# Optimization experiments

Hardware: AMD Instinct MI355X
Metric: run time of the kernel (lower is better)

The kernel has to match this reference:

```python
import jax, jax.numpy as jnp
import numpy as np

N = 262144   # faces = edges = vertices
E = 2000000  # connections per bipartite edge set
W = 32       # out_width


def _linear_block(x, w, b):
    # LinearBlock(in, out) with defaults -> Linear + LeakyReLU(0.01)
    return jax.nn.leaky_relu(x @ w + b)


def _bip_res_mr_conv(x_src, x_dst, e, w, b):
    # diffs = x_dst[e1] - x_src[e0]; scatter_max over dst; MLP(cat) residual
    diffs = x_dst[e[1]] - x_src[e[0]]                       # [E, W]
    maxes = jax.ops.segment_max(diffs, e[1], num_segments=x_dst.shape[0])
    # torch_scatter.scatter_max fills empty slots with 0
    maxes = jnp.where(jnp.isfinite(maxes), maxes, 0.0)
    h = _linear_block(jnp.concatenate([x_dst, maxes], axis=1), w, b)
    return x_dst + h


def setup_inputs() -> dict:
    key = jax.random.key(0)
    ks = jax.random.split(key, 16)
    inp = {
        "x_f": jax.random.normal(ks[0], (N, 4), dtype=jnp.float32),
        "x_e": jax.random.normal(ks[1], (N, 6), dtype=jnp.float32),
        "x_v": jax.random.normal(ks[2], (N, 3), dtype=jnp.float32),
        "e_fe": jax.random.randint(ks[3], (2, E), 0, N),
        "e_ev": jax.random.randint(ks[4], (2, E), 0, N),
        "e_ef": jax.random.randint(ks[5], (2, E), 0, N),
        "e_ve": jax.random.randint(ks[6], (2, E), 0, N),
    }
    def lin(k, cin, cout):
        s = 1.0 / np.sqrt(cin)
        kw, kb = jax.random.split(k)
        return (jax.random.uniform(kw, (cin, cout), minval=-s, maxval=s, dtype=jnp.float32),
                jax.random.uniform(kb, (cout,), minval=-s, maxval=s, dtype=jnp.float32))
    inp["wf"], inp["bf"] = lin(ks[7], 4, W)
    inp["we"], inp["be"] = lin(ks[8], 6, W)
    inp["wv"], inp["bv"] = lin(ks[9], 3, W)
    inp["w_f2e"], inp["b_f2e"] = lin(ks[10], 2 * W, W)
    inp["w_e2v"], inp["b_e2v"] = lin(ks[11], 2 * W, W)   # E2V conv
    return inp


def reference(x_f, x_e, x_v, e_fe, e_ev, e_ef, e_ve,
              wf, bf, we, be, wv, bv, w_f2e, b_f2e, w_e2v, b_e2v):
    x_f = _linear_block(x_f, wf, bf)
    x_e = _linear_block(x_e, we, be)
    x_v = _linear_block(x_v, wv, bv)
    # NB: original forward reuses self.F2E weights for three convs
    x_e = _bip_res_mr_conv(x_f, x_e, e_fe, w_f2e, b_f2e)
    x_v = _bip_res_mr_conv(x_e, x_v, e_ev, w_e2v, b_e2v)
    x_f = _bip_res_mr_conv(x_e, x_f, e_ef, w_f2e, b_f2e)
    x_e = _bip_res_mr_conv(x_v, x_e, e_ve, w_f2e, b_f2e)
    return (x_f, x_e, x_v)
```

## Files before the change

kernel.cpp:

```cpp
#include <hip/hip_runtime.h>
#include <hip/hip_fp16.h>
#include <math.h>

#define N_NODES 262144
#define NE      2000000
#define W_OUT   32

#define NBINS          2048
#define BIN_SHIFT      7
#define NPB            128
#define CAP            1200
#define MROW           33
#define MXU_DW         ((((NPB + 1) * MROW) + 3) & ~3)

__device__ __forceinline__ float lrelu(float x) { return x >= 0.f ? x : 0.01f * x; }

__device__ __forceinline__ unsigned short key16f(float r) {
    unsigned short u = __half_as_ushort(__float2half(r));
    return (u & 0x8000u) ? (unsigned short)(~u) : (unsigned short)(u | 0x8000u);
}
__device__ __forceinline__ float unkey16(unsigned k) {
    unsigned bits = (k & 0x8000u) ? (k ^ 0x8000u) : ((~k) & 0xFFFFu);
    return __half2float(__ushort_as_half((unsigned short)bits));
}
__device__ __forceinline__ unsigned fmin_key(float f) {
    unsigned u = __float_as_uint(f);
    return (u & 0x80000000u) ? ~u : (u | 0x80000000u);
}
__device__ __forceinline__ float fmin_unkey(unsigned u) {
    return __uint_as_float((u & 0x80000000u) ? (u ^ 0x80000000u) : ~u);
}

template<int K>
__global__ void proj_kernel(const float* __restrict__ x, const float* __restrict__ w,
                            const float* __restrict__ b, float* __restrict__ out,
                            unsigned short* __restrict__ out_k) {
    __shared__ float wl[K * 32];
    __shared__ float xl[8 * K];
    int t = threadIdx.x;
    for (int i = t; i < K * 32; i += 256) wl[i] = w[i];
    int nbase = blockIdx.x * 8;
    for (int i = t; i < 8 * K; i += 256) xl[i] = x[nbase * K + i];
    __syncthreads();
    int j = t & 31, ln = t >> 5;
    float acc = b[j];
#pragma unroll
    for (int k = 0; k < K; ++k) acc += xl[ln * K + k] * wl[k * 32 + j];
    float r = lrelu(acc);
    out[nbase * 32 + t] = r;
    if (out_k) out_k[nbase * 32 + t] = key16f(r);
}

__global__ __launch_bounds__(512)
void bin_pass3(const int* __restrict__ e0, const int* __restrict__ e1,
               int* __restrict__ gcur, unsigned int* __restrict__ buckets) {
    __shared__ unsigned int hist[NBINS];
    __shared__ unsigned int lcur[NBINS];
    __shared__ unsigned int gbase[NBINS];
    int t = threadIdx.x;
    for (int i = t; i < NBINS; i += 512) hist[i] = 0;
    __syncthreads();

    int q0 = blockIdx.x * 2048 + t;
    int4 d4[4];
#pragma unroll
    for (int k = 0; k < 4; ++k) {
        int q = q0 + k * 512;
        if (q < NE / 4) {
            d4[k] = ((const int4*)e1)[q];
            atomicAdd(&hist[((unsigned)d4[k].x) >> BIN_SHIFT], 1u);
            atomicAdd(&hist[((unsigned)d4[k].y) >> BIN_SHIFT], 1u);
            atomicAdd(&hist[((unsigned)d4[k].z) >> BIN_SHIFT], 1u);
            atomicAdd(&hist[((unsigned)d4[k].w) >> BIN_SHIFT], 1u);
        }
    }
    __syncthreads();
    for (int i = t; i < NBINS; i += 512) {
        lcur[i] = 0;
        if (hist[i]) gbase[i] = atomicAdd((unsigned int*)&gcur[i], hist[i]);
    }
    __syncthreads();
#pragma unroll
    for (int k = 0; k < 4; ++k) {
        int q = q0 + k * 512;
        if (q < NE / 4) {
            int4 s4 = ((const int4*)e0)[q];
            const int ds[4] = {d4[k].x, d4[k].y, d4[k].z, d4[k].w};
            const int ss[4] = {s4.x, s4.y, s4.z, s4.w};
#pragma unroll
            for (int j = 0; j < 4; ++j) {
                unsigned d = (unsigned)ds[j];
                unsigned bin = d >> BIN_SHIFT;
                unsigned pos = gbase[bin] + atomicAdd(&lcur[bin], 1u);
                if (pos < CAP)
                    buckets[(size_t)bin * CAP + pos] =
                        ((d & (NPB - 1u)) << 18) | (unsigned)ss[j];
            }
        }
    }
}

template<bool H>
__global__ __launch_bounds__(256)
void binreduce9(const int* __restrict__ gcur, const unsigned int* __restrict__ buckets,
                const void* __restrict__ srcv, const float* __restrict__ dst,
                const float* __restrict__ w, const float* __restrict__ b,
                float* __restrict__ out, unsigned short* __restrict__ out_k) {
    __shared__ unsigned mxu[MXU_DW];
    __shared__ __align__(16) float4 wl4[16 * 32];
    __shared__ __align__(16) float xmat[8][2][64];
    int t = threadIdx.x;
    int bin = blockIdx.x;
    int hw = t >> 5, c = t & 31;

    uint4* m4 = (uint4*)mxu;
    for (int i = t; i < MXU_DW / 4; i += 256)
        m4[i] = make_uint4(0xFFFFFFFFu, 0xFFFFFFFFu, 0xFFFFFFFFu, 0xFFFFFFFFu);
    for (int i = t; i < 512; i += 256) {
        int k4 = i >> 5, cc = i & 31;
        wl4[i] = make_float4(w[(k4 * 4 + 0) * 32 + cc], w[(k4 * 4 + 1) * 32 + cc],
                             w[(k4 * 4 + 2) * 32 + cc], w[(k4 * 4 + 3) * 32 + cc]);
    }
    __syncthreads();

    int nb = min(gcur[bin], CAP);
    const unsigned int* bk = buckets + (size_t)bin * CAP;
    const unsigned SENT = (unsigned)NPB << 18;
    const unsigned short* sk = (const unsigned short*)srcv;
    const float* sf = (const float*)srcv;
    for (int cbase = hw * 32; cbase < nb; cbase += 256) {
        int idx = cbase + c;
        unsigned ent = (idx < nb) ? bk[idx] : SENT;
#pragma unroll
        for (int k0 = 0; k0 < 32; k0 += 8) {
            unsigned v[8], nd[8];
#pragma unroll
            for (int j = 0; j < 8; ++j) {
                unsigned e = __shfl(ent, k0 + j, 32);
                nd[j] = e >> 18;
                size_t off = (size_t)(e & 0x3FFFFu) * 32 + c;
                if (H) v[j] = (unsigned)sk[off];
                else   v[j] = fmin_key(sf[off]);
            }
#pragma unroll
            for (int j = 0; j < 8; ++j)
                atomicMin(&mxu[nd[j] * MROW + c], v[j]);
        }
    }
    __syncthreads();

    float bc = b[c];
    size_t gb = (size_t)bin * NPB;
    for (int grp = 0; grp < 8; ++grp) {
        int n0 = hw * 16 + grp * 2;
#pragma unroll
        for (int gg = 0; gg < 2; ++gg) {
            int node = n0 + gg;
            float dv = dst[(gb + node) * 32 + c];
            unsigned mu = mxu[node * MROW + c];
            float mx;
            if (H) mx = (mu > 0xFFFFu) ? 0.0f : (dv - unkey16(mu));
            else   mx = (mu == 0xFFFFFFFFu) ? 0.0f : (dv - fmin_unkey(mu));
            xmat[hw][gg][c] = dv;
            xmat[hw][gg][32 + c] = mx;
        }
        __threadfence_block();

        float acc0 = bc, acc1 = bc;
#pragma unroll 4
        for (int k4 = 0; k4 < 16; ++k4) {
            float4 wv = wl4[k4 * 32 + c];
            float4 x0 = ((const float4*)xmat[hw][0])[k4];
            float4 x1 = ((const float4*)xmat[hw][1])[k4];
            acc0 += x0.x * wv.x + x0.y * wv.y + x0.z * wv.z + x0.w * wv.w;
            acc1 += x1.x * wv.x + x1.y * wv.y + x1.z * wv.z + x1.w * wv.w;
        }
        float r0 = xmat[hw][0][c] + lrelu(acc0);
        float r1 = xmat[hw][1][c] + lrelu(acc1);
        out[(gb + n0 + 0) * 32 + c] = r0;
        out[(gb + n0 + 1) * 32 + c] = r1;
        if (out_k) {
            out_k[(gb + n0 + 0) * 32 + c] = key16f(r0);
            out_k[(gb + n0 + 1) * 32 + c] = key16f(r1);
        }
        __threadfence_block();
    }
}

extern "C" void kernel_launch(void* const* d_in, const int* in_sizes, int n_in,
                              void* d_out, int out_size, void* d_ws, size_t ws_size,
                              hipStream_t stream) {
    const float* x_f  = (const float*)d_in[0];
    const float* x_e  = (const float*)d_in[1];
    const float* x_v  = (const float*)d_in[2];
    const int*   e_fe = (const int*)d_in[3];
    const int*   e_ev = (const int*)d_in[4];
    const int*   e_ef = (const int*)d_in[5];
    const int*   e_ve = (const int*)d_in[6];
    const float* wf    = (const float*)d_in[7];
    const float* bf    = (const float*)d_in[8];
    const float* we    = (const float*)d_in[9];
    const float* be    = (const float*)d_in[10];
    const float* wv    = (const float*)d_in[11];
    const float* bv    = (const float*)d_in[12];
    const float* w_f2e = (const float*)d_in[13];
    const float* b_f2e = (const float*)d_in[14];
    const float* w_e2v = (const float*)d_in[15];
    const float* b_e2v = (const float*)d_in[16];

    float* of = (float*)d_out;
    float* oe = of + (size_t)N_NODES * W_OUT;
    float* ov = oe + (size_t)N_NODES * W_OUT;

    const size_t NW = (size_t)N_NODES * W_OUT;

    float*          xe1     = (float*)d_ws;
    unsigned int*   buckets = (unsigned int*)(xe1 + NW);
    int*            gcur4   = (int*)(buckets + (size_t)NBINS * CAP);
    unsigned short* SA      = (unsigned short*)(gcur4 + 4 * NBINS);
    unsigned short* SB      = SA + NW;

    const size_t need = NW * 4 + (size_t)NBINS * CAP * 4 + 4 * NBINS * 4 + 2 * NW * 2;
    const bool useH = ws_size >= need;
    if (!useH) { SA = nullptr; SB = nullptr; }

    dim3 blk(256);
    const int bgrid = (NE / 4 + 2047) / 2048;

    (void)hipMemsetAsync(gcur4, 0, 4 * NBINS * sizeof(int), stream);

    proj_kernel<4><<<N_NODES / 8, blk, 0, stream>>>(x_f, wf, bf, of, SA);
    proj_kernel<6><<<N_NODES / 8, blk, 0, stream>>>(x_e, we, be, oe, nullptr);
    proj_kernel<3><<<N_NODES / 8, blk, 0, stream>>>(x_v, wv, bv, ov, nullptr);

    int conv_id = 0;
    auto conv = [&](const float* src, const unsigned short* src_k, const float* dstb,
                    const int* e, const float* w, const float* bias,
                    float* out, unsigned short* out_k) {
        int* gcur = gcur4 + conv_id * NBINS;
        ++conv_id;
        bin_pass3<<<bgrid, dim3(512), 0, stream>>>(e, e + NE, gcur, buckets);
        if (src_k)
            binreduce9<true><<<NBINS, blk, 0, stream>>>(gcur, buckets, (const void*)src_k,
                                                        dstb, w, bias, out, out_k);
        else
            binreduce9<false><<<NBINS, blk, 0, stream>>>(gcur, buckets, (const void*)src,
                                                         dstb, w, bias, out, out_k);
    };

    conv(of,  SA, oe, e_fe, w_f2e, b_f2e, xe1, SB);
    conv(xe1, SB, ov, e_ev, w_e2v, b_e2v, ov,  SA);
    conv(xe1, SB, of, e_ef, w_f2e, b_f2e, of,  nullptr);
    conv(ov,  SA, xe1, e_ve, w_f2e, b_f2e, oe, nullptr);
}
```

Measured before the change: 418.3 us.

## Software-pipeline gather loads ahead of LDS atomics and swizzle max table

The binned reduce kernel now issues the next batch of eight gathered source loads before running the atomicMin updates for the current batch, so global load latency overlaps the shared-memory atomics. The padded 33-wide shared max table is replaced by an XOR-swizzled 32-wide layout, which shrinks LDS use. Sentinel entries are masked to 0xFFFFFFFF instead of writing to an extra row. Launch bounds now request 6 blocks per CU, and the MLP epilogue processes one node per step instead of two. More live registers are needed for the double-buffered values, and the single-node epilogue gives up some reuse of the weight loads.

After: 458.2 us. +9.5%, slower.

```diff
diff --git a/kernel.cpp b/kernel.cpp
--- a/kernel.cpp
+++ b/kernel.cpp
@@ -10,8 +10,6 @@
 #define BIN_SHIFT      7
 #define NPB            128
 #define CAP            1200
-#define MROW           33
-#define MXU_DW         ((((NPB + 1) * MROW) + 3) & ~3)
 
 __device__ __forceinline__ float lrelu(float x) { return x >= 0.f ? x : 0.01f * x; }
 
@@ -30,6 +28,8 @@
 __device__ __forceinline__ float fmin_unkey(unsigned u) {
     return __uint_as_float((u & 0x80000000u) ? (u ^ 0x80000000u) : ~u);
 }
+
+#define MXIDX(nd, c) (((nd) << 5) + ((c) ^ ((nd) & 31u)))
 
 template<int K>
 __global__ void proj_kernel(const float* __restrict__ x, const float* __restrict__ w,
@@ -101,20 +101,20 @@
 }
 
 template<bool H>
-__global__ __launch_bounds__(256)
-void binreduce9(const int* __restrict__ gcur, const unsigned int* __restrict__ buckets,
-                const void* __restrict__ srcv, const float* __restrict__ dst,
-                const float* __restrict__ w, const float* __restrict__ b,
-                float* __restrict__ out, unsigned short* __restrict__ out_k) {
-    __shared__ unsigned mxu[MXU_DW];
+__global__ __launch_bounds__(256, 6)
+void binreduce10(const int* __restrict__ gcur, const unsigned int* __restrict__ buckets,
+                 const void* __restrict__ srcv, const float* __restrict__ dst,
+                 const float* __restrict__ w, const float* __restrict__ b,
+                 float* __restrict__ out, unsigned short* __restrict__ out_k) {
+    __shared__ unsigned mxu[NPB * 32];
     __shared__ __align__(16) float4 wl4[16 * 32];
-    __shared__ __align__(16) float xmat[8][2][64];
+    __shared__ __align__(16) float xmat[8][64];
     int t = threadIdx.x;
     int bin = blockIdx.x;
     int hw = t >> 5, c = t & 31;
 
     uint4* m4 = (uint4*)mxu;
-    for (int i = t; i < MXU_DW / 4; i += 256)
+    for (int i = t; i < NPB * 32 / 4; i += 256)
         m4[i] = make_uint4(0xFFFFFFFFu, 0xFFFFFFFFu, 0xFFFFFFFFu, 0xFFFFFFFFu);
     for (int i = t; i < 512; i += 256) {
         int k4 = i >> 5, cc = i & 31;
@@ -125,64 +125,69 @@
 
     int nb = min(gcur[bin], CAP);
     const unsigned int* bk = buckets + (size_t)bin * CAP;
-    const unsigned SENT = (unsigned)NPB << 18;
     const unsigned short* sk = (const unsigned short*)srcv;
     const float* sf = (const float*)srcv;
     for (int cbase = hw * 32; cbase < nb; cbase += 256) {
         int idx = cbase + c;
-        unsigned ent = (idx < nb) ? bk[idx] : SENT;
-#pragma unroll
-        for (int k0 = 0; k0 < 32; k0 += 8) {
-            unsigned v[8], nd[8];
-#pragma unroll
-            for (int j = 0; j < 8; ++j) {
-                unsigned e = __shfl(ent, k0 + j, 32);
-                nd[j] = e >> 18;
-                size_t off = (size_t)(e & 0x3FFFFu) * 32 + c;
-                if (H) v[j] = (unsigned)sk[off];
-                else   v[j] = fmin_key(sf[off]);
+        unsigned ent = (idx < nb) ? bk[idx] : 0xFFFFFFFFu;
+        unsigned va[8], aa[8];
+#pragma unroll
+        for (int j = 0; j < 8; ++j) {
+            unsigned e = __shfl(ent, j, 32);
+            unsigned nd = (e >> 18) & (NPB - 1u);
+            aa[j] = MXIDX(nd, (unsigned)c);
+            size_t off = (size_t)(e & 0x3FFFFu) * 32 + c;
+            unsigned lv = H ? (unsigned)sk[off] : fmin_key(sf[off]);
+            va[j] = (e >= (NPB << 18)) ? 0xFFFFFFFFu : lv;
+        }
+#pragma unroll
+        for (int k0 = 8; k0 <= 32; k0 += 8) {
+            unsigned vb[8], ab[8];
+            if (k0 < 32) {
+#pragma unroll
+                for (int j = 0; j < 8; ++j) {
+                    unsigned e = __shfl(ent, k0 + j, 32);
+                    unsigned nd = (e >> 18) & (NPB - 1u);
+                    ab[j] = MXIDX(nd, (unsigned)c);
+                    size_t off = (size_t)(e & 0x3FFFFu) * 32 + c;
+                    unsigned lv = H ? (unsigned)sk[off] : fmin_key(sf[off]);
+                    vb[j] = (e >= (NPB << 18)) ? 0xFFFFFFFFu : lv;
+                }
             }
 #pragma unroll
             for (int j = 0; j < 8; ++j)
-                atomicMin(&mxu[nd[j] * MROW + c], v[j]);
+                atomicMin(&mxu[aa[j]], va[j]);
+            if (k0 < 32) {
+#pragma unroll
+                for (int j = 0; j < 8; ++j) { va[j] = vb[j]; aa[j] = ab[j]; }
+            }
         }
     }
     __syncthreads();
 
     float bc = b[c];
     size_t gb = (size_t)bin * NPB;
-    for (int grp = 0; grp < 8; ++grp) {
-        int n0 = hw * 16 + grp * 2;
-#pragma unroll
-        for (int gg = 0; gg < 2; ++gg) {
-            int node = n0 + gg;
-            float dv = dst[(gb + node) * 32 + c];
-            unsigned mu = mxu[node * MROW + c];
-            float mx;
-            if (H) mx = (mu > 0xFFFFu) ? 0.0f : (dv - unkey16(mu));
-            else   mx = (mu == 0xFFFFFFFFu) ? 0.0f : (dv - fmin_unkey(mu));
-            xmat[hw][gg][c] = dv;
-            xmat[hw][gg][32 + c] = mx;
-        }
+    for (int grp = 0; grp < 16; ++grp) {
+        int node = hw * 16 + grp;
+        float dv = dst[(gb + node) * 32 + c];
+        unsigned mu = mxu[MXIDX((unsigned)node, (unsigned)c)];
+        float mx;
+        if (H) mx = (mu > 0xFFFFu) ? 0.0f : (dv - unkey16(mu));
+        else   mx = (mu == 0xFFFFFFFFu) ? 0.0f : (dv - fmin_unkey(mu));
+        xmat[hw][c] = dv;
+        xmat[hw][32 + c] = mx;
         __threadfence_block();
 
-        float acc0 = bc, acc1 = bc;
-#pragma unroll 4
+        float acc = bc;
+#pragma unroll
         for (int k4 = 0; k4 < 16; ++k4) {
             float4 wv = wl4[k4 * 32 + c];
-            float4 x0 = ((const float4*)xmat[hw][0])[k4];
-            float4 x1 = ((const float4*)xmat[hw][1])[k4];
-            acc0 += x0.x * wv.x + x0.y * wv.y + x0.z * wv.z + x0.w * wv.w;
-            acc1 += x1.x * wv.x + x1.y * wv.y + x1.z * wv.z + x1.w * wv.w;
-        }
-        float r0 = xmat[hw][0][c] + lrelu(acc0);
-        float r1 = xmat[hw][1][c] + lrelu(acc1);
-        out[(gb + n0 + 0) * 32 + c] = r0;
-        out[(gb + n0 + 1) * 32 + c] = r1;
-        if (out_k) {
-            out_k[(gb + n0 + 0) * 32 + c] = key16f(r0);
-            out_k[(gb + n0 + 1) * 32 + c] = key16f(r1);
-        }
+            float4 xv = ((const float4*)xmat[hw])[k4];
+            acc += xv.x * wv.x + xv.y * wv.y + xv.z * wv.z + xv.w * wv.w;
+        }
+        float r = dv + lrelu(acc);
+        out[(gb + node) * 32 + c] = r;
+        if (out_k) out_k[(gb + node) * 32 + c] = key16f(r);
         __threadfence_block();
     }
 }
@@ -241,11 +246,11 @@
         ++conv_id;
         bin_pass3<<<bgrid, dim3(512), 0, stream>>>(e, e + NE, gcur, buckets);
         if (src_k)
-            binreduce9<true><<<NBINS, blk, 0, stream>>>(gcur, buckets, (const void*)src_k,
-                                                        dstb, w, bias, out, out_k);
+            binreduce10<true><<<NBINS, blk, 0, stream>>>(gcur, buckets, (const void*)src_k,
+                                                         dstb, w, bias, out, out_k);
         else
-            binreduce9<false><<<NBINS, blk, 0, stream>>>(gcur, buckets, (const void*)src,
-                                                         dstb, w, bias, out, out_k);
+            binreduce10<false><<<NBINS, blk, 0, stream>>>(gcur, buckets, (const void*)src,
+                                                          dstb, w, bias, out, out_k);
     };
 
     conv(of,  SA, oe, e_fe, w_f2e, b_f2e, xe1, SB);
```
